# Performance work log

Measured on AMD Instinct MI355X. Metric: run time of the kernel, lower is better.

The kernel has to match this reference:

```python
import jax, jax.numpy as jnp
from jax import lax
import numpy as np

N, L, E, NHEAD, DFF = 16, 1024, 512, 8, 2048
HD = E // NHEAD
NLEVELS = 10  # log2(1024)
S_SCALES = NLEVELS + 1


def setup_inputs() -> dict:
    key = jax.random.key(0)
    ks = jax.random.split(key, 12)
    s = 0.05
    return {
        "src": jax.random.normal(ks[0], (N, L, E), jnp.float32),
        "conv_w": jax.random.normal(ks[1], (NLEVELS, HD, HD, 2), jnp.float32) * s,
        "conv_b": jax.random.normal(ks[2], (NLEVELS, HD), jnp.float32) * s,
        "in_proj_w": jax.random.normal(ks[3], (3 * E, E), jnp.float32) * s,
        "in_proj_b": jax.random.normal(ks[4], (3 * E,), jnp.float32) * s,
        "out_proj_w": jax.random.normal(ks[5], (E, E), jnp.float32) * s,
        "out_proj_b": jax.random.normal(ks[6], (E,), jnp.float32) * s,
        "ln1_w": jnp.ones((E,), jnp.float32),
        "ln1_b": jnp.zeros((E,), jnp.float32),
        "ln2_w": jnp.ones((E,), jnp.float32),
        "ln2_b": jnp.zeros((E,), jnp.float32),
        "w1": jax.random.normal(ks[7], (DFF, E), jnp.float32) * s,
        "b1": jax.random.normal(ks[8], (DFF,), jnp.float32) * s,
        "w2": jax.random.normal(ks[9], (E, DFF), jnp.float32) * s,
        "b2": jax.random.normal(ks[10], (E,), jnp.float32) * s,
    }


def _layer_norm(x, w, b, eps=1e-5):
    mu = jnp.mean(x, axis=-1, keepdims=True)
    var = jnp.mean(jnp.square(x - mu), axis=-1, keepdims=True)
    return (x - mu) * lax.rsqrt(var + eps) * w + b


def _forward(src, conv_w, conv_b, in_proj_w, in_proj_b, out_proj_w, out_proj_b,
             ln1_w, ln1_b, ln2_w, ln2_b, w1, b1, w2, b2):
    n, l, e = src.shape
    hd = e // NHEAD
    # pyramid over 1D spatial dim, channels-first
    out = jnp.transpose(src, (0, 2, 1))  # (N, E, L)
    hidden_vals = [out]
    for i in range(NLEVELS):
        x = out.reshape(n * NHEAD, hd, out.shape[-1])  # (N*H, hd, li)
        x = lax.conv_general_dilated(
            x, conv_w[i], window_strides=(2,), padding='VALID',
            dimension_numbers=('NCH', 'OIH', 'NCH'))
        x = jax.nn.relu(x + conv_b[i][None, :, None])
        out = x.reshape(n, e, x.shape[-1])  # (N, E, li/2)
        # upsample back to full length via repeat_interleave
        hidden_vals.append(jnp.repeat(out, l // out.shape[-1], axis=2))
    hv = jnp.stack(hidden_vals, -1)                      # (N, E, L, S)
    s = hv.shape[-1]
    hv = jnp.transpose(hv, (3, 0, 2, 1)).reshape(s, n * l, e)  # (S, N*L, E)

    # multi-head attention: length-1 query (finest scale) over all scales
    b_ = n * l
    q = hv[0:1] @ in_proj_w[:e].T + in_proj_b[:e]            # (1, B, E)
    k = hv @ in_proj_w[e:2 * e].T + in_proj_b[e:2 * e]       # (S, B, E)
    v = hv @ in_proj_w[2 * e:].T + in_proj_b[2 * e:]         # (S, B, E)
    qh = jnp.transpose(q.reshape(1, b_, NHEAD, hd), (1, 2, 0, 3))  # (B, H, 1, hd)
    kh = jnp.transpose(k.reshape(s, b_, NHEAD, hd), (1, 2, 0, 3))  # (B, H, S, hd)
    vh = jnp.transpose(v.reshape(s, b_, NHEAD, hd), (1, 2, 0, 3))  # (B, H, S, hd)
    scores = jnp.einsum('bhqd,bhkd->bhqk', qh, kh) / jnp.sqrt(jnp.float32(hd))
    attn = jax.nn.softmax(scores, axis=-1)
    o = jnp.einsum('bhqk,bhkd->bhqd', attn, vh)              # (B, H, 1, hd)
    o = o.reshape(b_, e) @ out_proj_w.T + out_proj_b         # (B, E)
    src2 = o.reshape(n, l, e)

    # faithful to source: residual computed then overwritten by norm1(src2)
    x = _layer_norm(src2, ln1_w, ln1_b)
    ff = jax.nn.relu(x @ w1.T + b1) @ w2.T + b2
    return _layer_norm(x + ff, ln2_w, ln2_b)


def reference(src, conv_w, conv_b, in_proj_w, in_proj_b, out_proj_w, out_proj_b,
              ln1_w, ln1_b, ln2_w, ln2_b, w1, b1, w2, b2):
    return _forward(src, conv_w, conv_b, in_proj_w, in_proj_b, out_proj_w,
                    out_proj_b, ln1_w, ln1_b, ln2_w, ln2_b, w1, b1, w2, b2)
```

## Files before the change

kernel.cpp:

```cpp
#include <hip/hip_runtime.h>
#include <hip/hip_bf16.h>
#include <stdint.h>
#include <math.h>

#define NB      16
#define LL      1024
#define EE      512
#define NHEADS  8
#define DFF     2048
#define NLEVELS 10
#define NSCALES 11
#define BROWS   (NB * LL)

typedef unsigned short u16;
typedef __attribute__((ext_vector_type(8))) short bf16x8;
typedef __attribute__((ext_vector_type(4))) float f32x4;

static const size_t B_SRCBF = 0;
static const size_t B_LVLBF = 16777216;
static const size_t B_QKV   = 33538048;
static const size_t B_KVS   = 83869696;
static const size_t B_OBF   = 117391360;
static const size_t B_XPRE  = 134168576;
static const size_t B_OUTBF = 150945792;
static const size_t B_XBF   = 167723008;
static const size_t B_WBF   = 184500224;
static const size_t B_FFH   = 0;

__device__ __forceinline__ u16 f2bf(float x) {
    union { float f; uint32_t u; } c; c.f = x;
    uint32_t u = c.u + 0x7FFFu + ((c.u >> 16) & 1u);
    return (u16)(u >> 16);
}
__device__ __forceinline__ float bf2f(u16 v) {
    union { uint32_t u; float f; } c; c.u = ((uint32_t)v) << 16; return c.f;
}
__device__ __forceinline__ uint32_t addbf2(uint32_t a, uint32_t b) {
    float lo = bf2f((u16)(a & 0xFFFF)) + bf2f((u16)(b & 0xFFFF));
    float hi = bf2f((u16)(a >> 16))    + bf2f((u16)(b >> 16));
    return (uint32_t)f2bf(lo) | ((uint32_t)f2bf(hi) << 16);
}
__device__ __forceinline__ void ld8bf(const u16* p, float* f) {
    uint4 r = *(const uint4*)p;
    uint32_t ws[4] = { r.x, r.y, r.z, r.w };
    #pragma unroll
    for (int j = 0; j < 4; j++) {
        union { uint32_t u; float g; } lo, hi;
        lo.u = ws[j] << 16; hi.u = ws[j] & 0xFFFF0000u;
        f[2 * j] = lo.g; f[2 * j + 1] = hi.g;
    }
}
__device__ __forceinline__ void gload16(const u16* g, u16* l) {
    __builtin_amdgcn_global_load_lds(
        (const __attribute__((address_space(1))) void*)g,
        (__attribute__((address_space(3))) void*)l, 16, 0, 0);
}

__global__ void cast_all_kernel(const float* __restrict__ s0, const float* __restrict__ s1,
                                const float* __restrict__ s2, const float* __restrict__ s3,
                                const float* __restrict__ s4, const float* __restrict__ cw,
                                u16* __restrict__ d0, u16* __restrict__ d1,
                                u16* __restrict__ d2, u16* __restrict__ d3,
                                u16* __restrict__ d4, u16* __restrict__ dw)
{
    int bid = blockIdx.x;
    if (bid >= 11264) {
        int base = (bid - 11264) * 1024 + threadIdx.x * 4;
        #pragma unroll
        for (int j = 0; j < 4; j++) {
            int idx = base + j;
            int lvl = idx >> 13, rem = idx & 8191;
            int o = rem >> 7, ck = rem & 127;
            int k = ck >> 6, ci = ck & 63;
            dw[idx] = f2bf(cw[(lvl << 13) + (o << 7) + (ci << 1) + k]);
        }
        return;
    }
    const float* s; u16* d; int nt;
    if      (bid < 8192)  { s = s0; d = d0; nt = 2097152; }
    else if (bid < 8960)  { bid -= 8192;  s = s1; d = d1; nt = 196608; }
    else if (bid < 9216)  { bid -= 8960;  s = s2; d = d2; nt = 65536;  }
    else if (bid < 10240) { bid -= 9216;  s = s3; d = d3; nt = 262144; }
    else                  { bid -= 10240; s = s4; d = d4; nt = 262144; }
    int i = bid * 256 + threadIdx.x;
    if (i < nt) {
        float4 v = ((const float4*)s)[i];
        uint2 o;
        o.x = (uint32_t)f2bf(v.x) | ((uint32_t)f2bf(v.y) << 16);
        o.y = (uint32_t)f2bf(v.z) | ((uint32_t)f2bf(v.w) << 16);
        ((uint2*)d)[i] = o;
    }
}

__global__ __launch_bounds__(256, 2)
void conv_chain_kernel(const u16* __restrict__ src_bf, u16* __restrict__ lvl_bf,
                       const u16* __restrict__ cw, const float* __restrict__ cb)
{
    __shared__ u16 BIG[16384];
    __shared__ u16 MID[8192];
    __shared__ u16 WB[8192];
    const int tid = threadIdx.x;
    const int l = tid & 63, w = tid >> 6;
    const int bid = blockIdx.x;
    const int q  = bid & 3;
    const int h  = (bid >> 2) & 7;
    const int n  = bid >> 5;

    {
        const u16* base = src_bf + ((size_t)n * 1024 + q * 256) * 512 + h * 64;
        #pragma unroll
        for (int j = 0; j < 8; j++) {
            int c = j * 256 + w * 64 + l;
            int row = c >> 3, lch = c & 7;
            int gch = lch ^ (row & 7);
            gload16(base + (size_t)row * 512 + gch * 8,
                    BIG + (size_t)(j * 256 + w * 64) * 8);
        }
    }

    const u16* IN = BIG;
    u16* OUTb = MID;
    int R = 128;
    int T = 512;
    size_t rowOff = 0;
    for (int lvl = 1; lvl <= 8; lvl++) {
        {
            const u16* wsrc = cw + (size_t)(lvl - 1) * 8192;
            #pragma unroll
            for (int j = 0; j < 4; j++) {
                int c = j * 256 + w * 64 + l;
                int o = c >> 4, lch = c & 15;
                int gch = lch ^ (o & 7);
                gload16(wsrc + o * 128 + gch * 8, WB + (size_t)(j * 256 + w * 64) * 8);
            }
        }
        asm volatile("s_waitcnt vmcnt(0)" ::: "memory");
        __syncthreads();

        const int nrt = (R + 15) >> 4;
        const int maxil = 2 * R - 1;
        for (int f = w; f < nrt * 4; f += 4) {
            int rt = f >> 2, nc = f & 3;
            int o = nc * 16 + (l & 15);
            f32x4 acc = {0.f, 0.f, 0.f, 0.f};
            #pragma unroll
            for (int s = 0; s < 4; s++) {
                int il = 2 * (rt * 16 + (l & 15)) + (s >> 1);
                if (il > maxil) il = maxil;
                int ach = (((s & 1) * 4) + (l >> 4)) ^ (il & 7);
                bf16x8 av = *(const bf16x8*)(IN + il * 64 + ach * 8);
                int bch = (s * 4 + (l >> 4)) ^ (o & 7);
                bf16x8 bv = *(const bf16x8*)(WB + o * 128 + bch * 8);
                acc = __builtin_amdgcn_mfma_f32_16x16x32_bf16(av, bv, acc, 0, 0, 0);
            }
            float bb = cb[(lvl - 1) * 64 + o];
            #pragma unroll
            for (int reg = 0; reg < 4; reg++) {
                int rloc = rt * 16 + (l >> 4) * 4 + reg;
                if (rloc < R) {
                    float v = fmaxf(acc[reg] + bb, 0.f);
                    u16 b16 = f2bf(v);
                    lvl_bf[(rowOff + (size_t)n * T + (size_t)q * R + rloc) * 512 + h * 64 + o] = b16;
                    OUTb[rloc * 64 + (((o >> 3) ^ (rloc & 7)) << 3) + (o & 7)] = b16;
                }
            }
        }
        __syncthreads();
        const u16* tmp = IN; IN = OUTb; OUTb = (u16*)tmp;
        rowOff += (size_t)16 * T;
        T >>= 1; R >>= 1;
    }
}

__global__ void conv_tail_kernel(u16* __restrict__ lvl_bf, const u16* __restrict__ cw,
                                 const float* __restrict__ cb)
{
    const int h = blockIdx.x & 7, n = blockIdx.x >> 3;
    const int tid = threadIdx.x;
    __shared__ float L8s[4][64];
    __shared__ float L9s[2][64];
    {
        int r = tid >> 6, c = tid & 63;
        L8s[r][c] = bf2f(lvl_bf[((size_t)16256 + n * 4 + r) * 512 + h * 64 + c]);
    }
    __syncthreads();
    if (tid < 128) {
        int t = tid >> 6, o = tid & 63;
        const u16* wr = cw + (size_t)8 * 8192 + o * 128;
        float acc = cb[8 * 64 + o];
        #pragma unroll
        for (int k = 0; k < 2; k++)
            #pragma unroll 16
            for (int ci = 0; ci < 64; ci++)
                acc += L8s[2 * t + k][ci] * bf2f(wr[k * 64 + ci]);
        acc = fmaxf(acc, 0.f);
        L9s[t][o] = acc;
        lvl_bf[((size_t)16320 + n * 2 + t) * 512 + h * 64 + o] = f2bf(acc);
    }
    __syncthreads();
    if (tid < 64) {
        int o = tid;
        const u16* wr = cw + (size_t)9 * 8192 + o * 128;
        float acc = cb[9 * 64 + o];
        #pragma unroll
        for (int k = 0; k < 2; k++)
            #pragma unroll 16
            for (int ci = 0; ci < 64; ci++)
                acc += L9s[k][ci] * bf2f(wr[k * 64 + ci]);
        acc = fmaxf(acc, 0.f);
        lvl_bf[((size_t)16352 + n) * 512 + h * 64 + o] = f2bf(acc);
    }
}

__global__ __launch_bounds__(512, 4)
void mfma_gemm(const u16* __restrict__ A, const u16* __restrict__ W,
               const float* __restrict__ bias,
               const u16* __restrict__ resb,
               u16* __restrict__ Cb,
               int M, int K, int N, int relu, int gx)
{
    __shared__ u16 lds[36864];
    const int tid = threadIdx.x;
    const int l = tid & 63, w = tid >> 6;
    const int wm = w >> 1, wn = w & 1;

    const int nwg = gridDim.x;
    const int q = nwg >> 3, r = nwg & 7;
    const int xcd = blockIdx.x & 7, idx = blockIdx.x >> 3;
    const int lin = (xcd < r ? xcd * (q + 1) : r * (q + 1) + (xcd - r) * q) + idx;
    const int by = lin / gx, bx = lin - by * gx;
    const int rowBase = by * 256, colBase = bx * 128;

    f32x4 acc[4][4];
    #pragma unroll
    for (int m = 0; m < 4; m++)
        #pragma unroll
        for (int n = 0; n < 4; n++) acc[m][n] = 0.f;

    const u16* gApt[2];
    const u16* gBpt;
    #pragma unroll
    for (int i = 0; i < 2; i++) {
        int G = i * 512 + tid;
        int row = G >> 2, p = G & 3;
        int c = p ^ ((row >> 1) & 3);
        int grow = rowBase + row; if (grow > M - 1) grow = M - 1;
        gApt[i] = A + (size_t)grow * K + c * 8;
    }
    {
        int G = tid;
        int row = G >> 2, p = G & 3;
        int c = p ^ ((row >> 1) & 3);
        gBpt = W + (size_t)(colBase + row) * K + c * 8;
    }

    const int NT = K >> 5;
    auto STAGE = [&](int tt, int buf) {
        const int kb = tt << 5;
        u16* dA = lds + buf * 12288;
        u16* dB = dA + 8192;
        gload16(gApt[0] + kb, dA + (size_t)(w * 64) * 8);
        gload16(gApt[1] + kb, dA + (size_t)(512 + w * 64) * 8);
        gload16(gBpt + kb, dB + (size_t)(w * 64) * 8);
    };
    STAGE(0, 0);
    if (NT > 1) STAGE(1, 1);

    int cbuf = 0, sbuf = 2;
    for (int t = 0; t < NT; ++t) {
        if (t + 1 < NT) asm volatile("s_waitcnt vmcnt(3)" ::: "memory");
        else            asm volatile("s_waitcnt vmcnt(0)" ::: "memory");
        __builtin_amdgcn_s_barrier();
        __builtin_amdgcn_sched_barrier(0);
        if (t + 2 < NT) STAGE(t + 2, sbuf);

        const u16* Ab = lds + cbuf * 12288;
        const u16* Bb = Ab + 8192;
        const int c = l >> 4;
        bf16x8 av[4], bv[4];
        #pragma unroll
        for (int fr = 0; fr < 4; fr++) {
            int row = wm * 64 + fr * 16 + (l & 15);
            av[fr] = *(const bf16x8*)(Ab + row * 32 + ((c ^ ((row >> 1) & 3)) * 8));
        }
        #pragma unroll
        for (int fc = 0; fc < 4; fc++) {
            int col = wn * 64 + fc * 16 + (l & 15);
            bv[fc] = *(const bf16x8*)(Bb + col * 32 + ((c ^ ((col >> 1) & 3)) * 8));
        }
        __builtin_amdgcn_s_setprio(1);
        #pragma unroll
        for (int m = 0; m < 4; m++)
            #pragma unroll
            for (int n = 0; n < 4; n++)
                acc[m][n] = __builtin_amdgcn_mfma_f32_16x16x32_bf16(av[m], bv[n], acc[m][n], 0, 0, 0);
        __builtin_amdgcn_s_setprio(0);

        cbuf = (cbuf == 2) ? 0 : cbuf + 1;
        sbuf = (sbuf == 2) ? 0 : sbuf + 1;
    }
    __builtin_amdgcn_s_barrier();
    __builtin_amdgcn_sched_barrier(0);

    const int cc = colBase + wn * 64 + (l & 15);
    float bs4[4];
    #pragma unroll
    for (int n = 0; n < 4; n++) bs4[n] = bias[cc + n * 16];

    u16* WS = lds + w * 2048;
    #pragma unroll
    for (int hh = 0; hh < 2; hh++) {
        #pragma unroll
        for (int mi = 0; mi < 2; mi++) {
            #pragma unroll
            for (int n = 0; n < 4; n++) {
                int colv = n * 16 + (l & 15);
                #pragma unroll
                for (int reg = 0; reg < 4; reg++) {
                    int rowh = mi * 16 + (l >> 4) * 4 + reg;
                    float v = acc[hh * 2 + mi][n][reg] + bs4[n];
                    if (relu) v = fmaxf(v, 0.f);
                    WS[rowh * 64 + (colv ^ (((rowh >> 2) & 3) << 4))] = f2bf(v);
                }
            }
        }
        asm volatile("s_waitcnt lgkmcnt(0)" ::: "memory");
        __builtin_amdgcn_sched_barrier(0);
        #pragma unroll
        for (int j = 0; j < 4; j++) {
            int rowh = (l >> 3) + 8 * j;
            int col8 = (l & 7) * 8;
            int colx = col8 ^ (((rowh >> 2) & 3) << 4);
            uint4 v = *(const uint4*)(WS + rowh * 64 + colx);
            int grow = rowBase + wm * 64 + hh * 32 + rowh;
            if (grow < M) {
                int gcol = colBase + wn * 64 + col8;
                if (resb) {
                    uint4 rb = *(const uint4*)&resb[(size_t)grow * N + gcol];
                    v.x = addbf2(v.x, rb.x);
                    v.y = addbf2(v.y, rb.y);
                    v.z = addbf2(v.z, rb.z);
                    v.w = addbf2(v.w, rb.w);
                }
                *(uint4*)(Cb + (size_t)grow * N + gcol) = v;
            }
        }
        asm volatile("s_waitcnt lgkmcnt(0)" ::: "memory");
    }
}

__global__ void attn_kernel(const u16* __restrict__ QKV, const u16* __restrict__ KVs,
                            u16* __restrict__ O)
{
    const int wv   = threadIdx.x >> 6;
    const int lane = threadIdx.x & 63;
    const int b    = blockIdx.x * 4 + wv;
    const int h    = lane >> 3;
    const int d8   = lane & 7;
    const int n = b >> 10, pos = b & 1023;

    float q[8];
    ld8bf(QKV + (size_t)b * 1536 + h * 64 + d8 * 8, q);

    float sc[NSCALES];
    {
        float kk[8];
        ld8bf(QKV + (size_t)b * 1536 + 512 + h * 64 + d8 * 8, kk);
        float p = 0.f;
        #pragma unroll
        for (int j = 0; j < 8; j++) p += q[j] * kk[j];
        p += __shfl_xor(p, 1); p += __shfl_xor(p, 2); p += __shfl_xor(p, 4);
        sc[0] = p * 0.125f;
    }
    {
        int rowOff = 0;
        #pragma unroll
        for (int s = 1; s <= NLEVELS; s++) {
            int Ls = 1024 >> s;
            int row = rowOff + n * Ls + (pos >> s);
            float kk[8];
            ld8bf(KVs + (size_t)row * 1024 + h * 64 + d8 * 8, kk);
            float p = 0.f;
            #pragma unroll
            for (int j = 0; j < 8; j++) p += q[j] * kk[j];
            p += __shfl_xor(p, 1); p += __shfl_xor(p, 2); p += __shfl_xor(p, 4);
            sc[s] = p * 0.125f;
            rowOff += 16 * Ls;
        }
    }
    float m = sc[0];
    #pragma unroll
    for (int s = 1; s < NSCALES; s++) m = fmaxf(m, sc[s]);
    float sum = 0.f;
    #pragma unroll
    for (int s = 0; s < NSCALES; s++) { sc[s] = __expf(sc[s] - m); sum += sc[s]; }
    float inv = 1.f / sum;

    float o[8] = {};
    {
        float vv[8];
        ld8bf(QKV + (size_t)b * 1536 + 1024 + h * 64 + d8 * 8, vv);
        float a = sc[0] * inv;
        #pragma unroll
        for (int j = 0; j < 8; j++) o[j] += a * vv[j];
    }
    {
        int rowOff = 0;
        #pragma unroll
        for (int s = 1; s <= NLEVELS; s++) {
            int Ls = 1024 >> s;
            int row = rowOff + n * Ls + (pos >> s);
            float vv[8];
            ld8bf(KVs + (size_t)row * 1024 + 512 + h * 64 + d8 * 8, vv);
            float a = sc[s] * inv;
            #pragma unroll
            for (int j = 0; j < 8; j++) o[j] += a * vv[j];
            rowOff += 16 * Ls;
        }
    }
    uint4 pk;
    pk.x = (uint32_t)f2bf(o[0]) | ((uint32_t)f2bf(o[1]) << 16);
    pk.y = (uint32_t)f2bf(o[2]) | ((uint32_t)f2bf(o[3]) << 16);
    pk.z = (uint32_t)f2bf(o[4]) | ((uint32_t)f2bf(o[5]) << 16);
    pk.w = (uint32_t)f2bf(o[6]) | ((uint32_t)f2bf(o[7]) << 16);
    *(uint4*)(O + (size_t)b * 512 + h * 64 + d8 * 8) = pk;
}

__global__ void ln_bf_kernel(const u16* __restrict__ in_bf,
                             const float* __restrict__ w, const float* __restrict__ b,
                             u16* __restrict__ out_bf, float* __restrict__ out_f)
{
    const int l = threadIdx.x & 63;
    const int row = blockIdx.x * 4 + (threadIdx.x >> 6);
    float v[8];
    ld8bf(in_bf + (size_t)row * EE + l * 8, v);
    float s = 0.f, s2 = 0.f;
    #pragma unroll
    for (int j = 0; j < 8; j++) { s += v[j]; s2 += v[j] * v[j]; }
    #pragma unroll
    for (int m = 1; m < 64; m <<= 1) { s += __shfl_xor(s, m); s2 += __shfl_xor(s2, m); }
    float mu  = s * (1.f / 512.f);
    float var = s2 * (1.f / 512.f) - mu * mu;
    float rs  = rsqrtf(var + 1e-5f);
    float4 w0 = *(const float4*)&w[l * 8], w1 = *(const float4*)&w[l * 8 + 4];
    float4 b0 = *(const float4*)&b[l * 8], b1 = *(const float4*)&b[l * 8 + 4];
    float o[8];
    o[0] = (v[0] - mu) * rs * w0.x + b0.x;
    o[1] = (v[1] - mu) * rs * w0.y + b0.y;
    o[2] = (v[2] - mu) * rs * w0.z + b0.z;
    o[3] = (v[3] - mu) * rs * w0.w + b0.w;
    o[4] = (v[4] - mu) * rs * w1.x + b1.x;
    o[5] = (v[5] - mu) * rs * w1.y + b1.y;
    o[6] = (v[6] - mu) * rs * w1.z + b1.z;
    o[7] = (v[7] - mu) * rs * w1.w + b1.w;
    if (out_bf) {
        uint4 pk;
        pk.x = (uint32_t)f2bf(o[0]) | ((uint32_t)f2bf(o[1]) << 16);
        pk.y = (uint32_t)f2bf(o[2]) | ((uint32_t)f2bf(o[3]) << 16);
        pk.z = (uint32_t)f2bf(o[4]) | ((uint32_t)f2bf(o[5]) << 16);
        pk.w = (uint32_t)f2bf(o[6]) | ((uint32_t)f2bf(o[7]) << 16);
        *(uint4*)(out_bf + (size_t)row * EE + l * 8) = pk;
    }
    if (out_f) {
        float* po = out_f + (size_t)row * EE + l * 8;
        *(float4*)po       = make_float4(o[0], o[1], o[2], o[3]);
        *(float4*)(po + 4) = make_float4(o[4], o[5], o[6], o[7]);
    }
}

extern "C" void kernel_launch(void* const* d_in, const int* in_sizes, int n_in,
                              void* d_out, int out_size, void* d_ws, size_t ws_size,
                              hipStream_t stream)
{
    const float* src        = (const float*)d_in[0];
    const float* conv_w     = (const float*)d_in[1];
    const float* conv_b     = (const float*)d_in[2];
    const float* in_proj_w  = (const float*)d_in[3];
    const float* in_proj_b  = (const float*)d_in[4];
    const float* out_proj_w = (const float*)d_in[5];
    const float* out_proj_b = (const float*)d_in[6];
    const float* ln1_w      = (const float*)d_in[7];
    const float* ln1_b      = (const float*)d_in[8];
    const float* ln2_w      = (const float*)d_in[9];
    const float* ln2_b      = (const float*)d_in[10];
    const float* w1         = (const float*)d_in[11];
    const float* b1         = (const float*)d_in[12];
    const float* w2         = (const float*)d_in[13];
    const float* b2         = (const float*)d_in[14];

    char*  wsb    = (char*)d_ws;
    float* out    = (float*)d_out;
    u16*   src_bf = (u16*)(wsb + B_SRCBF);
    u16*   lvl_bf = (u16*)(wsb + B_LVLBF);
    u16*   QKV    = (u16*)(wsb + B_QKV);
    u16*   KVs    = (u16*)(wsb + B_KVS);
    u16*   O_bf   = (u16*)(wsb + B_OBF);
    u16*   XPRE   = (u16*)(wsb + B_XPRE);
    u16*   OUTBF  = (u16*)(wsb + B_OUTBF);
    u16*   X_bf   = (u16*)(wsb + B_XBF);
    u16*   inw_bf = (u16*)(wsb + B_WBF);
    u16*   outw_bf= inw_bf + 786432;
    u16*   w1_bf  = outw_bf + 262144;
    u16*   w2_bf  = w1_bf + 1048576;
    u16*   cw_bf  = w2_bf + 1048576;
    u16*   FFH    = (u16*)(wsb + B_FFH);

    cast_all_kernel<<<11344, 256, 0, stream>>>(src, in_proj_w, out_proj_w, w1, w2, conv_w,
                                               src_bf, inw_bf, outw_bf, w1_bf, w2_bf, cw_bf);

    conv_chain_kernel<<<NB * NHEADS * 4, 256, 0, stream>>>(src_bf, lvl_bf, cw_bf, conv_b);
    conv_tail_kernel<<<NB * NHEADS, 256, 0, stream>>>(lvl_bf, cw_bf, conv_b);

    mfma_gemm<<<64 * 12, 512, 0, stream>>>(
        src_bf, inw_bf, in_proj_b, nullptr, QKV, BROWS, EE, 1536, 0, 12);

    mfma_gemm<<<64 * 8, 512, 0, stream>>>(
        lvl_bf, inw_bf + (size_t)512 * 512, in_proj_b + 512, nullptr, KVs,
        16368, EE, 1024, 0, 8);

    attn_kernel<<<BROWS / 4, 256, 0, stream>>>(QKV, KVs, O_bf);

    mfma_gemm<<<64 * 4, 512, 0, stream>>>(
        O_bf, outw_bf, out_proj_b, nullptr, XPRE, BROWS, EE, EE, 0, 4);

    ln_bf_kernel<<<BROWS / 4, 256, 0, stream>>>(XPRE, ln1_w, ln1_b, X_bf, nullptr);

    mfma_gemm<<<64 * 16, 512, 0, stream>>>(
        X_bf, w1_bf, b1, nullptr, FFH, BROWS, EE, DFF, 1, 16);

    mfma_gemm<<<64 * 4, 512, 0, stream>>>(
        FFH, w2_bf, b2, X_bf, OUTBF, BROWS, DFF, EE, 0, 4);

    ln_bf_kernel<<<BROWS / 4, 256, 0, stream>>>(OUTBF, ln2_w, ln2_b, nullptr, out);
}
```

Before: 234.7 us.

## Fuse LayerNorm into full-row GEMM epilogue for out-proj and FFN2

Result: no change. 236.1 us (+0.6%).

```diff
diff --git a/kernel.cpp b/kernel.cpp
--- a/kernel.cpp
+++ b/kernel.cpp
@@ -21,8 +21,6 @@
 static const size_t B_QKV   = 33538048;
 static const size_t B_KVS   = 83869696;
 static const size_t B_OBF   = 117391360;
-static const size_t B_XPRE  = 134168576;
-static const size_t B_OUTBF = 150945792;
 static const size_t B_XBF   = 167723008;
 static const size_t B_WBF   = 184500224;
 static const size_t B_FFH   = 0;
@@ -34,11 +32,6 @@
 }
 __device__ __forceinline__ float bf2f(u16 v) {
     union { uint32_t u; float f; } c; c.u = ((uint32_t)v) << 16; return c.f;
-}
-__device__ __forceinline__ uint32_t addbf2(uint32_t a, uint32_t b) {
-    float lo = bf2f((u16)(a & 0xFFFF)) + bf2f((u16)(b & 0xFFFF));
-    float hi = bf2f((u16)(a >> 16))    + bf2f((u16)(b >> 16));
-    return (uint32_t)f2bf(lo) | ((uint32_t)f2bf(hi) << 16);
 }
 __device__ __forceinline__ void ld8bf(const u16* p, float* f) {
     uint4 r = *(const uint4*)p;
@@ -215,7 +208,6 @@
 __global__ __launch_bounds__(512, 4)
 void mfma_gemm(const u16* __restrict__ A, const u16* __restrict__ W,
                const float* __restrict__ bias,
-               const u16* __restrict__ resb,
                u16* __restrict__ Cb,
                int M, int K, int N, int relu, int gx)
 {
@@ -333,19 +325,171 @@
             int colx = col8 ^ (((rowh >> 2) & 3) << 4);
             uint4 v = *(const uint4*)(WS + rowh * 64 + colx);
             int grow = rowBase + wm * 64 + hh * 32 + rowh;
-            if (grow < M) {
-                int gcol = colBase + wn * 64 + col8;
-                if (resb) {
-                    uint4 rb = *(const uint4*)&resb[(size_t)grow * N + gcol];
-                    v.x = addbf2(v.x, rb.x);
-                    v.y = addbf2(v.y, rb.y);
-                    v.z = addbf2(v.z, rb.z);
-                    v.w = addbf2(v.w, rb.w);
+            if (grow < M)
+                *(uint4*)(Cb + (size_t)grow * N + colBase + wn * 64 + col8) = v;
+        }
+        asm volatile("s_waitcnt lgkmcnt(0)" ::: "memory");
+    }
+}
+
+__global__ __launch_bounds__(512, 2)
+void mfma_gemm_ln(const u16* __restrict__ A, const u16* __restrict__ W,
+                  const float* __restrict__ bias, const u16* __restrict__ resb,
+                  const float* __restrict__ lnw, const float* __restrict__ lnb,
+                  u16* __restrict__ out_bf, float* __restrict__ out_f,
+                  int M, int K)
+{
+    __shared__ u16 lds[55296];
+    const int tid = threadIdx.x;
+    const int l = tid & 63, w = tid >> 6;
+
+    const int nwg = gridDim.x;
+    const int q = nwg >> 3, r = nwg & 7;
+    const int xcd = blockIdx.x & 7, idx = blockIdx.x >> 3;
+    const int by = (xcd < r ? xcd * (q + 1) : r * (q + 1) + (xcd - r) * q) + idx;
+    const int rowBase = by * 64;
+
+    f32x4 acc[4][4];
+    #pragma unroll
+    for (int m = 0; m < 4; m++)
+        #pragma unroll
+        for (int n = 0; n < 4; n++) acc[m][n] = 0.f;
+
+    const u16* gApt = nullptr;
+    const u16* gBpt[4];
+    if (tid < 256) {
+        int row = tid >> 2, p = tid & 3;
+        int c = p ^ ((row >> 1) & 3);
+        gApt = A + (size_t)(rowBase + row) * K + c * 8;
+    }
+    #pragma unroll
+    for (int j = 0; j < 4; j++) {
+        int G = j * 512 + tid;
+        int row = G >> 2, p = G & 3;
+        int c = p ^ ((row >> 1) & 3);
+        gBpt[j] = W + (size_t)row * K + c * 8;
+    }
+
+    const int NT = K >> 5;
+    auto STAGE = [&](int tt, int buf) {
+        const int kb = tt << 5;
+        u16* dA = lds + buf * 18432;
+        u16* dB = dA + 2048;
+        if (w < 4) gload16(gApt + kb, dA + (size_t)(w * 64) * 8);
+        #pragma unroll
+        for (int j = 0; j < 4; j++)
+            gload16(gBpt[j] + kb, dB + (size_t)(j * 512 + w * 64) * 8);
+    };
+    STAGE(0, 0);
+    if (NT > 1) STAGE(1, 1);
+
+    int cbuf = 0, sbuf = 2;
+    for (int t = 0; t < NT; ++t) {
+        if (t + 1 < NT) {
+            if (w < 4) asm volatile("s_waitcnt vmcnt(5)" ::: "memory");
+            else       asm volatile("s_waitcnt vmcnt(4)" ::: "memory");
+        } else {
+            asm volatile("s_waitcnt vmcnt(0)" ::: "memory");
+        }
+        __builtin_amdgcn_s_barrier();
+        __builtin_amdgcn_sched_barrier(0);
+        if (t + 2 < NT) STAGE(t + 2, sbuf);
+
+        const u16* Ab = lds + cbuf * 18432;
+        const u16* Bb = Ab + 2048;
+        const int c = l >> 4;
+        bf16x8 av[4], bv[4];
+        #pragma unroll
+        for (int fr = 0; fr < 4; fr++) {
+            int row = fr * 16 + (l & 15);
+            av[fr] = *(const bf16x8*)(Ab + row * 32 + ((c ^ ((row >> 1) & 3)) * 8));
+        }
+        #pragma unroll
+        for (int fc = 0; fc < 4; fc++) {
+            int col = w * 64 + fc * 16 + (l & 15);
+            bv[fc] = *(const bf16x8*)(Bb + col * 32 + ((c ^ ((col >> 1) & 3)) * 8));
+        }
+        __builtin_amdgcn_s_setprio(1);
+        #pragma unroll
+        for (int m = 0; m < 4; m++)
+            #pragma unroll
+            for (int n = 0; n < 4; n++)
+                acc[m][n] = __builtin_amdgcn_mfma_f32_16x16x32_bf16(av[m], bv[n], acc[m][n], 0, 0, 0);
+        __builtin_amdgcn_s_setprio(0);
+
+        cbuf = (cbuf == 2) ? 0 : cbuf + 1;
+        sbuf = (sbuf == 2) ? 0 : sbuf + 1;
+    }
+    __builtin_amdgcn_s_barrier();
+    __builtin_amdgcn_sched_barrier(0);
+
+    {
+        const int cbase = w * 64 + (l & 15);
+        float bs4[4];
+        #pragma unroll
+        for (int n = 0; n < 4; n++) bs4[n] = bias[cbase + n * 16];
+        #pragma unroll
+        for (int m = 0; m < 4; m++) {
+            #pragma unroll
+            for (int n = 0; n < 4; n++) {
+                int col = cbase + n * 16;
+                #pragma unroll
+                for (int reg = 0; reg < 4; reg++) {
+                    int row = m * 16 + (l >> 4) * 4 + reg;
+                    float v = acc[m][n][reg] + bs4[n];
+                    lds[row * 512 + (col ^ ((row & 7) << 3))] = f2bf(v);
                 }
-                *(uint4*)(Cb + (size_t)grow * N + gcol) = v;
             }
         }
-        asm volatile("s_waitcnt lgkmcnt(0)" ::: "memory");
+    }
+    __syncthreads();
+
+    float w0a = lnw[l * 8 + 0], w1a = lnw[l * 8 + 1], w2a = lnw[l * 8 + 2], w3a = lnw[l * 8 + 3];
+    float w4a = lnw[l * 8 + 4], w5a = lnw[l * 8 + 5], w6a = lnw[l * 8 + 6], w7a = lnw[l * 8 + 7];
+    float b0a = lnb[l * 8 + 0], b1a = lnb[l * 8 + 1], b2a = lnb[l * 8 + 2], b3a = lnb[l * 8 + 3];
+    float b4a = lnb[l * 8 + 4], b5a = lnb[l * 8 + 5], b6a = lnb[l * 8 + 6], b7a = lnb[l * 8 + 7];
+
+    for (int rr = 0; rr < 8; rr++) {
+        int row = w * 8 + rr;
+        int grow = rowBase + row;
+        float v[8];
+        ld8bf(lds + row * 512 + (((l ^ (row & 7)) * 8)), v);
+        if (resb) {
+            float vr[8];
+            ld8bf(resb + (size_t)grow * EE + l * 8, vr);
+            #pragma unroll
+            for (int j = 0; j < 8; j++) v[j] += vr[j];
+        }
+        float s = 0.f, s2 = 0.f;
+        #pragma unroll
+        for (int j = 0; j < 8; j++) { s += v[j]; s2 += v[j] * v[j]; }
+        #pragma unroll
+        for (int m = 1; m < 64; m <<= 1) { s += __shfl_xor(s, m); s2 += __shfl_xor(s2, m); }
+        float mu  = s * (1.f / 512.f);
+        float var = s2 * (1.f / 512.f) - mu * mu;
+        float rs  = rsqrtf(var + 1e-5f);
+        float o[8];
+        o[0] = (v[0] - mu) * rs * w0a + b0a;
+        o[1] = (v[1] - mu) * rs * w1a + b1a;
+        o[2] = (v[2] - mu) * rs * w2a + b2a;
+        o[3] = (v[3] - mu) * rs * w3a + b3a;
+        o[4] = (v[4] - mu) * rs * w4a + b4a;
+        o[5] = (v[5] - mu) * rs * w5a + b5a;
+        o[6] = (v[6] - mu) * rs * w6a + b6a;
+        o[7] = (v[7] - mu) * rs * w7a + b7a;
+        if (out_bf) {
+            uint4 pk;
+            pk.x = (uint32_t)f2bf(o[0]) | ((uint32_t)f2bf(o[1]) << 16);
+            pk.y = (uint32_t)f2bf(o[2]) | ((uint32_t)f2bf(o[3]) << 16);
+            pk.z = (uint32_t)f2bf(o[4]) | ((uint32_t)f2bf(o[5]) << 16);
+            pk.w = (uint32_t)f2bf(o[6]) | ((uint32_t)f2bf(o[7]) << 16);
+            *(uint4*)(out_bf + (size_t)grow * EE + l * 8) = pk;
+        }
+        if (out_f) {
+            float* po = out_f + (size_t)grow * EE + l * 8;
+            *(float4*)po       = make_float4(o[0], o[1], o[2], o[3]);
+            *(float4*)(po + 4) = make_float4(o[4], o[5], o[6], o[7]);
+        }
     }
 }
 
@@ -424,48 +568,6 @@
     pk.z = (uint32_t)f2bf(o[4]) | ((uint32_t)f2bf(o[5]) << 16);
     pk.w = (uint32_t)f2bf(o[6]) | ((uint32_t)f2bf(o[7]) << 16);
     *(uint4*)(O + (size_t)b * 512 + h * 64 + d8 * 8) = pk;
-}
-
-__global__ void ln_bf_kernel(const u16* __restrict__ in_bf,
-                             const float* __restrict__ w, const float* __restrict__ b,
-                             u16* __restrict__ out_bf, float* __restrict__ out_f)
-{
-    const int l = threadIdx.x & 63;
-    const int row = blockIdx.x * 4 + (threadIdx.x >> 6);
-    float v[8];
-    ld8bf(in_bf + (size_t)row * EE + l * 8, v);
-    float s = 0.f, s2 = 0.f;
-    #pragma unroll
-    for (int j = 0; j < 8; j++) { s += v[j]; s2 += v[j] * v[j]; }
-    #pragma unroll
-    for (int m = 1; m < 64; m <<= 1) { s += __shfl_xor(s, m); s2 += __shfl_xor(s2, m); }
-    float mu  = s * (1.f / 512.f);
-    float var = s2 * (1.f / 512.f) - mu * mu;
-    float rs  = rsqrtf(var + 1e-5f);
-    float4 w0 = *(const float4*)&w[l * 8], w1 = *(const float4*)&w[l * 8 + 4];
-    float4 b0 = *(const float4*)&b[l * 8], b1 = *(const float4*)&b[l * 8 + 4];
-    float o[8];
-    o[0] = (v[0] - mu) * rs * w0.x + b0.x;
-    o[1] = (v[1] - mu) * rs * w0.y + b0.y;
-    o[2] = (v[2] - mu) * rs * w0.z + b0.z;
-    o[3] = (v[3] - mu) * rs * w0.w + b0.w;
-    o[4] = (v[4] - mu) * rs * w1.x + b1.x;
-    o[5] = (v[5] - mu) * rs * w1.y + b1.y;
-    o[6] = (v[6] - mu) * rs * w1.z + b1.z;
-    o[7] = (v[7] - mu) * rs * w1.w + b1.w;
-    if (out_bf) {
-        uint4 pk;
-        pk.x = (uint32_t)f2bf(o[0]) | ((uint32_t)f2bf(o[1]) << 16);
-        pk.y = (uint32_t)f2bf(o[2]) | ((uint32_t)f2bf(o[3]) << 16);
-        pk.z = (uint32_t)f2bf(o[4]) | ((uint32_t)f2bf(o[5]) << 16);
-        pk.w = (uint32_t)f2bf(o[6]) | ((uint32_t)f2bf(o[7]) << 16);
-        *(uint4*)(out_bf + (size_t)row * EE + l * 8) = pk;
-    }
-    if (out_f) {
-        float* po = out_f + (size_t)row * EE + l * 8;
-        *(float4*)po       = make_float4(o[0], o[1], o[2], o[3]);
-        *(float4*)(po + 4) = make_float4(o[4], o[5], o[6], o[7]);
-    }
 }
 
 extern "C" void kernel_launch(void* const* d_in, const int* in_sizes, int n_in,
@@ -495,8 +597,6 @@
     u16*   QKV    = (u16*)(wsb + B_QKV);
     u16*   KVs    = (u16*)(wsb + B_KVS);
     u16*   O_bf   = (u16*)(wsb + B_OBF);
-    u16*   XPRE   = (u16*)(wsb + B_XPRE);
-    u16*   OUTBF  = (u16*)(wsb + B_OUTBF);
     u16*   X_bf   = (u16*)(wsb + B_XBF);
     u16*   inw_bf = (u16*)(wsb + B_WBF);
     u16*   outw_bf= inw_bf + 786432;
@@ -512,24 +612,20 @@
     conv_tail_kernel<<<NB * NHEADS, 256, 0, stream>>>(lvl_bf, cw_bf, conv_b);
 
     mfma_gemm<<<64 * 12, 512, 0, stream>>>(
-        src_bf, inw_bf, in_proj_b, nullptr, QKV, BROWS, EE, 1536, 0, 12);
+        src_bf, inw_bf, in_proj_b, QKV, BROWS, EE, 1536, 0, 12);
 
     mfma_gemm<<<64 * 8, 512, 0, stream>>>(
-        lvl_bf, inw_bf + (size_t)512 * 512, in_proj_b + 512, nullptr, KVs,
+        lvl_bf, inw_bf + (size_t)512 * 512, in_proj_b + 512, KVs,
         16368, EE, 1024, 0, 8);
 
     attn_kernel<<<BROWS / 4, 256, 0, stream>>>(QKV, KVs, O_bf);
 
-    mfma_gemm<<<64 * 4, 512, 0, stream>>>(
-        O_bf, outw_bf, out_proj_b, nullptr, XPRE, BROWS, EE, EE, 0, 4);
-
-    ln_bf_kernel<<<BROWS / 4, 256, 0, stream>>>(XPRE, ln1_w, ln1_b, X_bf, nullptr);
+    mfma_gemm_ln<<<256, 512, 0, stream>>>(
+        O_bf, outw_bf, out_proj_b, nullptr, ln1_w, ln1_b, X_bf, nullptr, BROWS, EE);
 
     mfma_gemm<<<64 * 16, 512, 0, stream>>>(
-        X_bf, w1_bf, b1, nullptr, FFH, BROWS, EE, DFF, 1, 16);
-
-    mfma_gemm<<<64 * 4, 512, 0, stream>>>(
-        FFH, w2_bf, b2, X_bf, OUTBF, BROWS, DFF, EE, 0, 4);
-
-    ln_bf_kernel<<<BROWS / 4, 256, 0, stream>>>(OUTBF, ln2_w, ln2_b, nullptr, out);
-}
+        X_bf, w1_bf, b1, FFH, BROWS, EE, DFF, 1, 16);
+
+    mfma_gemm_ln<<<256, 512, 0, stream>>>(
+        FFH, w2_bf, b2, X_bf, ln2_w, ln2_b, nullptr, out, BROWS, DFF);
+}
```
